# Optimization experiments

Measured on AMD Instinct MI355X. Metric: run time of the kernel, lower is better.

## Reference

```python
import jax, jax.numpy as jnp
import numpy as np

B, Q, D, H, HD, P = 1, 2048, 2048, 16, 128, 512


def setup_inputs() -> dict:
    key = jax.random.key(0)
    ks = jax.random.split(key, 12)
    x = jax.random.normal(ks[0], (B, Q, D), jnp.float32)
    prefix_key = jax.random.normal(ks[1], (B, P, H, HD), jnp.float32)
    prefix_value = jax.random.normal(ks[2], (B, P, H, HD), jnp.float32)
    s = 1.0 / np.sqrt(D)
    Wq = jax.random.normal(ks[3], (D, H, HD), jnp.float32) * s
    Wk = jax.random.normal(ks[4], (D, H, HD), jnp.float32) * s
    Wv = jax.random.normal(ks[5], (D, H, HD), jnp.float32) * s
    bq = jnp.zeros((H, HD), jnp.float32)
    bk = jnp.zeros((H, HD), jnp.float32)
    bv = jnp.zeros((H, HD), jnp.float32)
    prefix_gate = jax.random.normal(ks[6], (H,), jnp.float32) * 0.1
    Wout = jax.random.normal(ks[7], (H, HD, D), jnp.float32) * (1.0 / np.sqrt(D))
    bout = jnp.zeros((D,), jnp.float32)
    # prefix fully visible, causal mask over the suffix (current sequence)
    causal = jnp.tril(jnp.ones((Q, Q), bool))
    mask = jnp.concatenate([jnp.ones((Q, P), bool), causal], axis=1)[None, None]  # [1,1,Q,P+Q]
    return dict(x=x, prefix_key=prefix_key, prefix_value=prefix_value,
                Wq=Wq, bq=bq, Wk=Wk, bk=bk, Wv=Wv, bv=bv,
                prefix_gate=prefix_gate, Wout=Wout, bout=bout, mask=mask)


def reference(x, prefix_key, prefix_value, Wq, bq, Wk, bk, Wv, bv, prefix_gate, Wout, bout, mask):
    head_dim = Wq.shape[-1]
    pl = prefix_key.shape[1]
    q = jnp.einsum('bqd,dhk->bqhk', x, Wq) + bq   # [B,Q,H,HD]
    k = jnp.einsum('bqd,dhk->bqhk', x, Wk) + bk
    v = jnp.einsum('bqd,dhk->bqhk', x, Wv) + bv
    k = jnp.concatenate([prefix_key, k], axis=1)   # [B,P+Q,H,HD]
    v = jnp.concatenate([prefix_value, v], axis=1)
    q = q / jnp.sqrt(jnp.asarray(head_dim, q.dtype))
    w = jnp.einsum('bqhd,bkhd->bhqk', q, k)        # [B,H,Q,P+Q]
    big_neg = jnp.finfo(w.dtype).min
    w = jnp.where(mask, w, big_neg)
    gate = prefix_gate[None, :, None, None]
    w_prefix = jax.nn.softmax(w[..., :pl]) * gate   # gated prefix segment
    w_suffix = jax.nn.softmax(w[..., pl:])          # regular suffix softmax
    w = jnp.concatenate([w_prefix, w_suffix], axis=-1)
    o = jnp.einsum('bhqk,bkhd->bqhd', w, v)         # [B,Q,H,HD]
    return jnp.einsum('bqhd,hdo->bqo', o, Wout) + bout
```

## Files before the change

### kernel.cpp

```cpp
#include <hip/hip_runtime.h>
#include <hip/hip_bf16.h>

typedef __bf16 bf16x8 __attribute__((ext_vector_type(8)));
typedef __bf16 bf16x4v __attribute__((ext_vector_type(4)));
typedef float f32x4 __attribute__((ext_vector_type(4)));

#define DMODEL 2048
#define NH 16
#define HD 128
#define PLEN 512
#define QLEN 2048
#define KVLEN 2560

__device__ __forceinline__ void gload_lds16(const void* g, void* l) {
  __builtin_amdgcn_global_load_lds((const __attribute__((address_space(1))) void*)g,
                                   (__attribute__((address_space(3))) void*)l, 16, 0, 0);
}

__device__ __forceinline__ unsigned cvt_pk_bf16(float lo, float hi) {
  unsigned r;
  asm volatile("v_cvt_pk_bf16_f32 %0, %1, %2" : "=v"(r) : "v"(lo), "v"(hi));
  return r;
}

__global__ __launch_bounds__(256) void k_prep(const float* __restrict__ Wq,
                                              const float* __restrict__ Wk,
                                              const float* __restrict__ Wv,
                                              const float* __restrict__ Wo,
                                              const float* __restrict__ x,
                                              const float* __restrict__ pk,
                                              const float* __restrict__ pv,
                                              __bf16* __restrict__ WqT,
                                              __bf16* __restrict__ WkT,
                                              __bf16* __restrict__ WvT,
                                              __bf16* __restrict__ WoT,
                                              __bf16* __restrict__ xb,
                                              __bf16* __restrict__ Kall,
                                              __bf16* __restrict__ VT) {
  __shared__ float tile[64][65];
  const int z = blockIdx.z;
  const int t = threadIdx.x;
  const int tx = t & 63, ty = t >> 6;
  if (z < 4) {
    const float* in = (z == 0) ? Wq : (z == 1) ? Wk : (z == 2) ? Wv : Wo;
    __bf16* out = (z == 0) ? WqT : (z == 1) ? WkT : (z == 2) ? WvT : WoT;
    const int r0 = blockIdx.y * 64, c0 = blockIdx.x * 64;
#pragma unroll
    for (int i = 0; i < 16; ++i) {
      int r = ty + i * 4;
      tile[r][tx] = in[(size_t)(r0 + r) * DMODEL + c0 + tx];
    }
    __syncthreads();
#pragma unroll
    for (int i = 0; i < 16; ++i) {
      int r = ty + i * 4;
      out[(size_t)(c0 + r) * DMODEL + r0 + tx] = (__bf16)tile[tx][r];
    }
  } else if (z == 4) {
    const int r0 = blockIdx.y * 64, c0 = blockIdx.x * 64;
#pragma unroll
    for (int i = 0; i < 16; ++i) {
      int r = ty + i * 4;
      xb[(size_t)(r0 + r) * DMODEL + c0 + tx] = (__bf16)x[(size_t)(r0 + r) * DMODEL + c0 + tx];
    }
  } else {
    const int blk = blockIdx.y * 32 + blockIdx.x;
#pragma unroll
    for (int i = 0; i < 4; ++i) {
      int idx = blk * 1024 + i * 256 + t;
      int hd = idx & 127;
      int hh = (idx >> 7) & 15;
      int p = idx >> 11;
      Kall[(size_t)hh * KVLEN * HD + (size_t)p * HD + hd] = (__bf16)pk[idx];
      VT[(size_t)hh * HD * KVLEN + (size_t)hd * KVLEN + p] = (__bf16)pv[idx];
    }
  }
}


template <int BN>
__device__ __forceinline__ void stage_tile(const __bf16* __restrict__ A,
                                           const __bf16* __restrict__ BT,
                                           char* AsmB, char* BsmB,
                                           int m0, int n0, int k0, int w, int l) {
#pragma unroll
  for (int i = 0; i < 2; ++i) {
    int base = i * 4096 + w * 1024;
    int o = base + l * 16;
    int row = o >> 6, col = (o & 63) >> 1;
    gload_lds16(A + (size_t)(m0 + row) * DMODEL + k0 + col, AsmB + base);
  }
  if constexpr (BN == 128) {
#pragma unroll
    for (int i = 0; i < 2; ++i) {
      int base = i * 4096 + w * 1024;
      int o = base + l * 16;
      int row = o >> 6, col = (o & 63) >> 1;
      gload_lds16(BT + (size_t)(n0 + row) * DMODEL + k0 + col, BsmB + base);
    }
  } else {
    int base = w * 1024;
    int o = base + l * 16;
    int row = o >> 6, col = (o & 63) >> 1;
    gload_lds16(BT + (size_t)(n0 + row) * DMODEL + k0 + col, BsmB + base);
  }
}

template <int BN>
__device__ __forceinline__ void gemm_mainloop_db(const __bf16* __restrict__ A,
                                                 const __bf16* __restrict__ BT,
                                                 __bf16* Asm, __bf16* Bsm,
                                                 int m0, int n0, int w, int l,
                                                 f32x4 (&acc)[4][BN / 32]) {
  constexpr int NI = BN / 32;
  constexpr int ABUF = 4096;
  constexpr int BBUF = BN * 32;
  const int lr = l & 15, lg = l >> 4;
  int cur = 0;
  stage_tile<BN>(A, BT, (char*)Asm, (char*)Bsm, m0, n0, 0, w, l);
  __syncthreads();
  for (int k0 = 0; k0 < DMODEL; k0 += 32) {
    if (k0 + 32 < DMODEL)
      stage_tile<BN>(A, BT, (char*)(Asm + (cur ^ 1) * ABUF), (char*)(Bsm + (cur ^ 1) * BBUF),
                     m0, n0, k0 + 32, w, l);
    const __bf16* Ab = Asm + cur * ABUF;
    const __bf16* Bb = Bsm + cur * BBUF;
    bf16x8 af[4], bfv[NI];
#pragma unroll
    for (int mi = 0; mi < 4; ++mi)
      af[mi] = *(const bf16x8*)(Ab + ((w >> 1) * 64 + mi * 16 + lr) * 32 + lg * 8);
#pragma unroll
    for (int ni = 0; ni < NI; ++ni)
      bfv[ni] = *(const bf16x8*)(Bb + ((w & 1) * (BN / 2) + ni * 16 + lr) * 32 + lg * 8);
    __builtin_amdgcn_s_setprio(1);
#pragma unroll
    for (int mi = 0; mi < 4; ++mi)
#pragma unroll
      for (int ni = 0; ni < NI; ++ni)
        acc[mi][ni] = __builtin_amdgcn_mfma_f32_16x16x32_bf16(af[mi], bfv[ni], acc[mi][ni], 0, 0, 0);
    __builtin_amdgcn_s_setprio(0);
    __syncthreads();
    cur ^= 1;
  }
}

__global__ __launch_bounds__(256) void gemm_qkv(const __bf16* __restrict__ xb,
                                                const __bf16* __restrict__ WqT,
                                                const __bf16* __restrict__ WkT,
                                                const __bf16* __restrict__ WvT,
                                                const float* __restrict__ bq,
                                                const float* __restrict__ bk,
                                                const float* __restrict__ bv,
                                                __bf16* __restrict__ Qs,
                                                __bf16* __restrict__ Kall,
                                                __bf16* __restrict__ VT) {
  __shared__ __bf16 Asm[2][4096];
  __shared__ __bf16 Bsm[2][4096];
  const int t = threadIdx.x, w = t >> 6, l = t & 63;
  const int m0 = blockIdx.x * 128, n0 = blockIdx.y * 128;
  const int z = blockIdx.z;
  const __bf16* BT = (z == 0) ? WqT : ((z == 1) ? WkT : WvT);
  const float* bias = (z == 0) ? bq : ((z == 1) ? bk : bv);
  f32x4 acc[4][4];
#pragma unroll
  for (int mi = 0; mi < 4; ++mi)
#pragma unroll
    for (int ni = 0; ni < 4; ++ni) acc[mi][ni] = (f32x4){0.f, 0.f, 0.f, 0.f};
  gemm_mainloop_db<128>(xb, BT, &Asm[0][0], &Bsm[0][0], m0, n0, w, l, acc);
  const int lr = l & 15, lg = l >> 4;
#pragma unroll
  for (int mi = 0; mi < 4; ++mi)
#pragma unroll
    for (int ni = 0; ni < 4; ++ni)
#pragma unroll
      for (int r = 0; r < 4; ++r) {
        int row = m0 + (w >> 1) * 64 + mi * 16 + lg * 4 + r;
        int col = n0 + (w & 1) * 64 + ni * 16 + lr;
        float v = acc[mi][ni][r] + bias[col];
        int hh = col >> 7, hd = col & 127;
        if (z == 0) {
          Qs[(size_t)hh * QLEN * HD + (size_t)row * HD + hd] = (__bf16)(v * 0.08838834764831845f);
        } else if (z == 1) {
          Kall[(size_t)hh * KVLEN * HD + (size_t)(PLEN + row) * HD + hd] = (__bf16)v;
        } else {
          VT[(size_t)hh * HD * KVLEN + (size_t)hd * KVLEN + (PLEN + row)] = (__bf16)v;
        }
      }
}

__global__ __launch_bounds__(256) void gemm_out(const __bf16* __restrict__ Ob,
                                                const __bf16* __restrict__ WoT,
                                                const float* __restrict__ bout,
                                                float* __restrict__ out) {
  __shared__ __bf16 Asm[2][4096];
  __shared__ __bf16 Bsm[2][2048];
  const int t = threadIdx.x, w = t >> 6, l = t & 63;
  const int m0 = blockIdx.x * 128, n0 = blockIdx.y * 64;
  f32x4 acc[4][2];
#pragma unroll
  for (int mi = 0; mi < 4; ++mi)
#pragma unroll
    for (int ni = 0; ni < 2; ++ni) acc[mi][ni] = (f32x4){0.f, 0.f, 0.f, 0.f};
  gemm_mainloop_db<64>(Ob, WoT, &Asm[0][0], &Bsm[0][0], m0, n0, w, l, acc);
  const int lr = l & 15, lg = l >> 4;
#pragma unroll
  for (int mi = 0; mi < 4; ++mi)
#pragma unroll
    for (int ni = 0; ni < 2; ++ni)
#pragma unroll
      for (int r = 0; r < 4; ++r) {
        int row = m0 + (w >> 1) * 64 + mi * 16 + lg * 4 + r;
        int col = n0 + (w & 1) * 32 + ni * 16 + lr;
        out[(size_t)row * DMODEL + col] = acc[mi][ni][r] + bout[col];
      }
}

template <int KS>
__global__ __launch_bounds__(256, 4) void k_attn(const __bf16* __restrict__ Qs,
                                                 const __bf16* __restrict__ Kall,
                                                 const __bf16* __restrict__ VT,
                                                 __bf16* __restrict__ P1buf,
                                                 float* __restrict__ S1buf,
                                                 __bf16* __restrict__ P2buf,
                                                 float* __restrict__ S2buf) {
  __shared__ __bf16 Ksm[2][4096];
  __shared__ __bf16 Vsm[2][4096];
  const int id = blockIdx.x;
  const int b = id & 255, k = id >> 8;
  const int h = b >> 4, m = b & 15;
  int qt, z;
  if constexpr (KS == 2) {
    z = k >> 1;
    const int j = 2 * m + (k >> 1);
    qt = (k & 1) ? (31 - j) : j;
  } else {
    z = 0;
    qt = (k & 1) ? (31 - 2 * m) : (2 * m);
  }
  const int t = threadIdx.x, w = t >> 6, l = t & 63;
  const int lr = l & 15, lg = l >> 4;
  const int q0 = qt * 64 + w * 16;
  const __bf16* Qh = Qs + (size_t)h * QLEN * HD;
  const char* Khb = (const char*)(Kall + (size_t)h * KVLEN * HD);
  const char* Vhb = (const char*)(VT + (size_t)h * HD * KVLEN);

  bf16x8 qf[4];
#pragma unroll
  for (int c = 0; c < 4; ++c)
    qf[c] = *(const bf16x8*)(Qh + (size_t)(q0 + lr) * HD + c * 32 + lg * 8);

  f32x4 acc[8];
  float ss;

  auto STAGE = [&](int buf, int kb) {
#pragma unroll
    for (int i = 0; i < 2; ++i) {
      int o = (i * 256 + w * 64 + l) * 16;
      int po = o ^ (((o >> 8) & 7) << 4);
      gload_lds16(Khb + (size_t)kb * 256 + po, (char*)&Ksm[buf][0] + i * 4096 + w * 1024);
    }
#pragma unroll
    for (int i = 0; i < 2; ++i) {
      int o = (i * 256 + w * 64 + l) * 16;
      int po = o ^ (((o >> 7) & 7) << 4);
      int row = po >> 6, colb = po & 63;
      gload_lds16(Vhb + (size_t)row * (KVLEN * 2) + (size_t)kb * 2 + colb,
                  (char*)&Vsm[buf][0] + i * 4096 + w * 1024);
    }
  };

  auto COMPUTE = [&](int buf, int mrel, bool domask) {
    const char* Kb = (const char*)&Ksm[buf][0];
    const char* Vb = (const char*)&Vsm[buf][0];
    f32x4 st0 = {0.f, 0.f, 0.f, 0.f}, st1 = {0.f, 0.f, 0.f, 0.f};
    __builtin_amdgcn_s_setprio(1);
#pragma unroll
    for (int c = 0; c < 4; ++c) {
      int o0 = lr * 256 + c * 64 + lg * 16;        o0 ^= ((o0 >> 8) & 7) << 4;
      int o1 = (16 + lr) * 256 + c * 64 + lg * 16; o1 ^= ((o1 >> 8) & 7) << 4;
      bf16x8 kf0 = *(const bf16x8*)(Kb + o0);
      bf16x8 kf1 = *(const bf16x8*)(Kb + o1);
      st0 = __builtin_amdgcn_mfma_f32_16x16x32_bf16(kf0, qf[c], st0, 0, 0, 0);
      st1 = __builtin_amdgcn_mfma_f32_16x16x32_bf16(kf1, qf[c], st1, 0, 0, 0);
    }
    __builtin_amdgcn_s_setprio(0);
    const int qabs = q0 + lr;
    float e0[4], e1[4];
    float ps = 0.f;
#pragma unroll
    for (int r = 0; r < 4; ++r) {
      e0[r] = __expf(st0[r] - 16.0f);
      e1[r] = __expf(st1[r] - 16.0f);
      if (domask) {
        if (mrel + 4 * lg + r > qabs) e0[r] = 0.f;
        if (mrel + 16 + 4 * lg + r > qabs) e1[r] = 0.f;
      }
      ps += e0[r] + e1[r];
    }
    ss += ps;
    unsigned W0 = cvt_pk_bf16(e0[0], e0[1]);
    unsigned W1 = cvt_pk_bf16(e0[2], e0[3]);
    unsigned W2 = cvt_pk_bf16(e1[0], e1[1]);
    unsigned W3 = cvt_pk_bf16(e1[2], e1[3]);
    const int srcA = lr + (((2 * lg) & 3) << 4);
    const int srcB = lr + (((2 * lg + 1) & 3) << 4);
    unsigned A0 = __shfl(W0, srcA), A1 = __shfl(W1, srcA);
    unsigned A2 = __shfl(W0, srcB), A3 = __shfl(W1, srcB);
    unsigned B0 = __shfl(W2, srcA), B1 = __shfl(W3, srcA);
    unsigned B2 = __shfl(W2, srcB), B3 = __shfl(W3, srcB);
    union { unsigned u[4]; bf16x8 v; } pu;
    pu.u[0] = (lg < 2) ? A0 : B0;
    pu.u[1] = (lg < 2) ? A1 : B1;
    pu.u[2] = (lg < 2) ? A2 : B2;
    pu.u[3] = (lg < 2) ? A3 : B3;
    bf16x8 pf = pu.v;
    __builtin_amdgcn_s_setprio(1);
#pragma unroll
    for (int c = 0; c < 8; ++c) {
      int o = (c * 16 + lr) * 64 + lg * 16; o ^= ((o >> 7) & 7) << 4;
      bf16x8 vf = *(const bf16x8*)(Vb + o);
      acc[c] = __builtin_amdgcn_mfma_f32_16x16x32_bf16(pf, vf, acc[c], 0, 0, 0);
    }
    __builtin_amdgcn_s_setprio(0);
  };

  auto STORE_PHASE = [&](__bf16* PBUF, float* SBUF) {
    const size_t rb = (size_t)(z * NH + h) * QLEN;
    float s = ss;
    s += __shfl_xor(s, 16);
    s += __shfl_xor(s, 32);
    if (l < 16) SBUF[rb + q0 + l] = s;
#pragma unroll
    for (int r = 0; r < 4; ++r) {
      const int row = q0 + lg * 4 + r;
#pragma unroll
      for (int c = 0; c < 8; ++c)
        PBUF[(rb + row) * HD + c * 16 + lr] = (__bf16)acc[c][r];
    }
  };

#pragma unroll
  for (int c = 0; c < 8; ++c) acc[c] = (f32x4){0.f, 0.f, 0.f, 0.f};
  ss = 0.f;
  int cur = 0;
  STAGE(0, z * 32);
  __syncthreads();
#pragma unroll 1
  for (int tt = z; tt < 16; tt += KS) {
    if (tt + KS < 16) STAGE(cur ^ 1, (tt + KS) * 32);
    else STAGE(cur ^ 1, PLEN + z * 32);
    COMPUTE(cur, 0, false);
    __syncthreads();
    cur ^= 1;
  }
  STORE_PHASE(P1buf, S1buf);

#pragma unroll
  for (int c = 0; c < 8; ++c) acc[c] = (f32x4){0.f, 0.f, 0.f, 0.f};
  ss = 0.f;
  const int ntb = 2 * qt + 2;
#pragma unroll 1
  for (int tt = z; tt < ntb; tt += KS) {
    if (tt + KS < ntb) STAGE(cur ^ 1, PLEN + (tt + KS) * 32);
    COMPUTE(cur, tt * 32, tt * 32 + 31 > q0);
    __syncthreads();
    cur ^= 1;
  }
  STORE_PHASE(P2buf, S2buf);
}

template <int KS>
__global__ __launch_bounds__(256) void k_combine(const __bf16* __restrict__ P1buf,
                                                 const float* __restrict__ S1buf,
                                                 const __bf16* __restrict__ P2buf,
                                                 const float* __restrict__ S2buf,
                                                 const float* __restrict__ gate,
                                                 __bf16* __restrict__ Ob) {
  const int idx = blockIdx.x * 256 + threadIdx.x;
  const int d = idx & 127;
  const int q = (idx >> 7) & 2047;
  const int h = idx >> 18;
  const size_t rq = (size_t)h * QLEN + q;
  float a1 = 0.f, a2 = 0.f, s1 = 0.f, s2 = 0.f;
#pragma unroll
  for (int zz = 0; zz < KS; ++zz) {
    const size_t zb = (size_t)zz * NH * QLEN;
    a1 += (float)P1buf[(zb + rq) * HD + d];
    a2 += (float)P2buf[(zb + rq) * HD + d];
    s1 += S1buf[zb + rq];
    s2 += S2buf[zb + rq];
  }
  float o = a1 * (gate[h] / s1) + a2 / s2;
  Ob[(size_t)q * DMODEL + h * HD + d] = (__bf16)o;
}


extern "C" void kernel_launch(void* const* d_in, const int* in_sizes, int n_in,
                              void* d_out, int out_size, void* d_ws, size_t ws_size,
                              hipStream_t stream) {
  const float* x    = (const float*)d_in[0];
  const float* pk   = (const float*)d_in[1];
  const float* pv   = (const float*)d_in[2];
  const float* Wq   = (const float*)d_in[3];
  const float* bq   = (const float*)d_in[4];
  const float* Wk   = (const float*)d_in[5];
  const float* bk   = (const float*)d_in[6];
  const float* Wv   = (const float*)d_in[7];
  const float* bv   = (const float*)d_in[8];
  const float* gate = (const float*)d_in[9];
  const float* Wout = (const float*)d_in[10];
  const float* bout = (const float*)d_in[11];
  float* out = (float*)d_out;

  char* ws = (char*)d_ws;
  size_t off = 0;
  auto alc = [&](size_t bytes) -> char* {
    char* p = ws + off;
    off += bytes;
    off = (off + 255) & ~(size_t)255;
    return p;
  };
  __bf16* xb   = (__bf16*)alc((size_t)DMODEL * DMODEL * 2);
  __bf16* WqT  = (__bf16*)alc((size_t)DMODEL * DMODEL * 2);
  __bf16* WkT  = (__bf16*)alc((size_t)DMODEL * DMODEL * 2);
  __bf16* WvT  = (__bf16*)alc((size_t)DMODEL * DMODEL * 2);
  __bf16* WoT  = (__bf16*)alc((size_t)DMODEL * DMODEL * 2);
  __bf16* Qs   = (__bf16*)alc((size_t)NH * QLEN * HD * 2);
  __bf16* Kall = (__bf16*)alc((size_t)NH * KVLEN * HD * 2);
  __bf16* VTa  = (__bf16*)alc((size_t)NH * HD * KVLEN * 2);
  __bf16* Ob   = (__bf16*)alc((size_t)QLEN * DMODEL * 2);

  const size_t per_split = (size_t)NH * QLEN * HD * 2 * 2
                         + (size_t)NH * QLEN * 4 * 2 + 1024;
  int KS = (off + 2 * per_split <= ws_size) ? 2 : 1;
  __bf16* P1buf = (__bf16*)alc((size_t)KS * NH * QLEN * HD * 2);
  __bf16* P2buf = (__bf16*)alc((size_t)KS * NH * QLEN * HD * 2);
  float*  S1buf = (float*)alc((size_t)KS * NH * QLEN * 4);
  float*  S2buf = (float*)alc((size_t)KS * NH * QLEN * 4);

  k_prep<<<dim3(32, 32, 6), 256, 0, stream>>>(Wq, Wk, Wv, Wout, x, pk, pv,
                                              WqT, WkT, WvT, WoT, xb, Kall, VTa);

  gemm_qkv<<<dim3(16, 16, 3), 256, 0, stream>>>(xb, WqT, WkT, WvT, bq, bk, bv, Qs, Kall, VTa);

  const int ncomb = (NH * QLEN * HD) / 256;
  if (KS == 2) {
    k_attn<2><<<1024, 256, 0, stream>>>(Qs, Kall, VTa, P1buf, S1buf, P2buf, S2buf);
    k_combine<2><<<ncomb, 256, 0, stream>>>(P1buf, S1buf, P2buf, S2buf, gate, Ob);
  } else {
    k_attn<1><<<512, 256, 0, stream>>>(Qs, Kall, VTa, P1buf, S1buf, P2buf, S2buf);
    k_combine<1><<<ncomb, 256, 0, stream>>>(P1buf, S1buf, P2buf, S2buf, gate, Ob);
  }
  gemm_out<<<dim3(16, 32), 256, 0, stream>>>(Ob, WoT, bout, out);
}
```

Measured before the change: 194.3 us.

## Move Wout transpose and prefix K/V conversion into QKV GEMM launch

The Wout transpose and the prefix key/value bf16 conversion move out of the prep kernel and run as an extra z-slice of the QKV GEMM grid. That work can then overlap with the GEMM blocks and shortens the prep kernel on the critical path. The prefix V transpose now goes through an LDS tile so that writes to VT are coalesced instead of strided scalar stores. The extra blocks compete with the GEMM blocks for CUs, and the LDS is unified into one buffer to share space.

```diff
diff --git a/kernel.cpp b/kernel.cpp
--- a/kernel.cpp
+++ b/kernel.cpp
@@ -2,7 +2,6 @@
 #include <hip/hip_bf16.h>
 
 typedef __bf16 bf16x8 __attribute__((ext_vector_type(8)));
-typedef __bf16 bf16x4v __attribute__((ext_vector_type(4)));
 typedef float f32x4 __attribute__((ext_vector_type(4)));
 
 #define DMODEL 2048
@@ -26,25 +25,19 @@
 __global__ __launch_bounds__(256) void k_prep(const float* __restrict__ Wq,
                                               const float* __restrict__ Wk,
                                               const float* __restrict__ Wv,
-                                              const float* __restrict__ Wo,
                                               const float* __restrict__ x,
-                                              const float* __restrict__ pk,
-                                              const float* __restrict__ pv,
                                               __bf16* __restrict__ WqT,
                                               __bf16* __restrict__ WkT,
                                               __bf16* __restrict__ WvT,
-                                              __bf16* __restrict__ WoT,
-                                              __bf16* __restrict__ xb,
-                                              __bf16* __restrict__ Kall,
-                                              __bf16* __restrict__ VT) {
+                                              __bf16* __restrict__ xb) {
   __shared__ float tile[64][65];
   const int z = blockIdx.z;
   const int t = threadIdx.x;
   const int tx = t & 63, ty = t >> 6;
-  if (z < 4) {
-    const float* in = (z == 0) ? Wq : (z == 1) ? Wk : (z == 2) ? Wv : Wo;
-    __bf16* out = (z == 0) ? WqT : (z == 1) ? WkT : (z == 2) ? WvT : WoT;
-    const int r0 = blockIdx.y * 64, c0 = blockIdx.x * 64;
+  const int r0 = blockIdx.y * 64, c0 = blockIdx.x * 64;
+  if (z < 3) {
+    const float* in = (z == 0) ? Wq : (z == 1) ? Wk : Wv;
+    __bf16* out = (z == 0) ? WqT : (z == 1) ? WkT : WvT;
 #pragma unroll
     for (int i = 0; i < 16; ++i) {
       int r = ty + i * 4;
@@ -56,23 +49,11 @@
       int r = ty + i * 4;
       out[(size_t)(c0 + r) * DMODEL + r0 + tx] = (__bf16)tile[tx][r];
     }
-  } else if (z == 4) {
-    const int r0 = blockIdx.y * 64, c0 = blockIdx.x * 64;
+  } else {
 #pragma unroll
     for (int i = 0; i < 16; ++i) {
       int r = ty + i * 4;
       xb[(size_t)(r0 + r) * DMODEL + c0 + tx] = (__bf16)x[(size_t)(r0 + r) * DMODEL + c0 + tx];
-    }
-  } else {
-    const int blk = blockIdx.y * 32 + blockIdx.x;
-#pragma unroll
-    for (int i = 0; i < 4; ++i) {
-      int idx = blk * 1024 + i * 256 + t;
-      int hd = idx & 127;
-      int hh = (idx >> 7) & 15;
-      int p = idx >> 11;
-      Kall[(size_t)hh * KVLEN * HD + (size_t)p * HD + hd] = (__bf16)pk[idx];
-      VT[(size_t)hh * HD * KVLEN + (size_t)hd * KVLEN + p] = (__bf16)pv[idx];
     }
   }
 }
@@ -151,14 +132,70 @@
                                                 const float* __restrict__ bq,
                                                 const float* __restrict__ bk,
                                                 const float* __restrict__ bv,
+                                                const float* __restrict__ Wo,
+                                                const float* __restrict__ pk,
+                                                const float* __restrict__ pv,
                                                 __bf16* __restrict__ Qs,
                                                 __bf16* __restrict__ Kall,
-                                                __bf16* __restrict__ VT) {
-  __shared__ __bf16 Asm[2][4096];
-  __shared__ __bf16 Bsm[2][4096];
+                                                __bf16* __restrict__ VT,
+                                                __bf16* __restrict__ WoT) {
+  __shared__ __bf16 smem[16384];
   const int t = threadIdx.x, w = t >> 6, l = t & 63;
+  const int z = blockIdx.z;
+
+  if (z == 3) {
+    const int b = blockIdx.y * 16 + blockIdx.x;
+    float* tile = (float*)smem;
+    const int tx = t & 63, ty = t >> 6;
+#pragma unroll 1
+    for (int tt = 0; tt < 4; ++tt) {
+      const int tid = b * 4 + tt;
+      const int r0 = (tid >> 5) * 64, c0 = (tid & 31) * 64;
+      __syncthreads();
+#pragma unroll
+      for (int i = 0; i < 16; ++i) {
+        int r = ty + i * 4;
+        tile[r * 65 + tx] = Wo[(size_t)(r0 + r) * DMODEL + c0 + tx];
+      }
+      __syncthreads();
+#pragma unroll
+      for (int i = 0; i < 16; ++i) {
+        int r = ty + i * 4;
+        WoT[(size_t)(c0 + r) * DMODEL + r0 + tx] = (__bf16)tile[tx * 65 + r];
+      }
+    }
+#pragma unroll
+    for (int i = 0; i < 16; ++i) {
+      int idx = b * 4096 + i * 256 + t;
+      int hd = idx & 127, hh = (idx >> 7) & 15, p = idx >> 11;
+      Kall[(size_t)hh * KVLEN * HD + (size_t)p * HD + hd] = (__bf16)pk[idx];
+    }
+    if (b < 128) {
+      __bf16* Vt = smem;
+      const int h = b >> 3, p0 = (b & 7) * 64;
+      __syncthreads();
+#pragma unroll
+      for (int i = 0; i < 32; ++i) {
+        int idx = i * 256 + t;
+        int hd = idx & 127, p = idx >> 7;
+        Vt[hd * 66 + p] = (__bf16)pv[(size_t)(p0 + p) * DMODEL + h * HD + hd];
+      }
+      __syncthreads();
+      if (l < 32) {
+#pragma unroll
+        for (int j = 0; j < 32; ++j) {
+          int hd = w * 32 + j;
+          unsigned u = *(const unsigned*)&Vt[hd * 66 + 2 * l];
+          *(unsigned*)(VT + (size_t)h * HD * KVLEN + (size_t)hd * KVLEN + p0 + 2 * l) = u;
+        }
+      }
+    }
+    return;
+  }
+
+  __bf16* Asm = smem;
+  __bf16* Bsm = smem + 8192;
   const int m0 = blockIdx.x * 128, n0 = blockIdx.y * 128;
-  const int z = blockIdx.z;
   const __bf16* BT = (z == 0) ? WqT : ((z == 1) ? WkT : WvT);
   const float* bias = (z == 0) ? bq : ((z == 1) ? bk : bv);
   f32x4 acc[4][4];
@@ -166,7 +203,7 @@
   for (int mi = 0; mi < 4; ++mi)
 #pragma unroll
     for (int ni = 0; ni < 4; ++ni) acc[mi][ni] = (f32x4){0.f, 0.f, 0.f, 0.f};
-  gemm_mainloop_db<128>(xb, BT, &Asm[0][0], &Bsm[0][0], m0, n0, w, l, acc);
+  gemm_mainloop_db<128>(xb, BT, Asm, Bsm, m0, n0, w, l, acc);
   const int lr = l & 15, lg = l >> 4;
 #pragma unroll
   for (int mi = 0; mi < 4; ++mi)
@@ -438,10 +475,10 @@
   float*  S1buf = (float*)alc((size_t)KS * NH * QLEN * 4);
   float*  S2buf = (float*)alc((size_t)KS * NH * QLEN * 4);
 
-  k_prep<<<dim3(32, 32, 6), 256, 0, stream>>>(Wq, Wk, Wv, Wout, x, pk, pv,
-                                              WqT, WkT, WvT, WoT, xb, Kall, VTa);
-
-  gemm_qkv<<<dim3(16, 16, 3), 256, 0, stream>>>(xb, WqT, WkT, WvT, bq, bk, bv, Qs, Kall, VTa);
+  k_prep<<<dim3(32, 32, 4), 256, 0, stream>>>(Wq, Wk, Wv, x, WqT, WkT, WvT, xb);
+
+  gemm_qkv<<<dim3(16, 16, 4), 256, 0, stream>>>(xb, WqT, WkT, WvT, bq, bk, bv,
+                                                Wout, pk, pv, Qs, Kall, VTa, WoT);
 
   const int ncomb = (NH * QLEN * HD) / 256;
   if (KS == 2) {
```

Measured after the change: 197.0 us. No clear change (+1.4%).
